# Kernel optimization log

Measured on AMD Instinct MI355X. Metric: run time of the kernel, lower is better.

The kernel has to match this reference:

```python
import jax, jax.numpy as jnp
import numpy as np
from jax import lax

B, CIN, COUT, K = 256, 3, 16, 3
D, H, W_ = 16, 32, 32
POOL = 4


def setup_inputs() -> dict:
    key = jax.random.key(0)
    kx, kw, kb = jax.random.split(key, 3)
    x = jax.random.normal(kx, (B, CIN, D, H, W_), dtype=jnp.float32)
    # Conv3d default init scale ~ 1/sqrt(fan_in)
    fan_in = CIN * K * K * K
    bound = 1.0 / np.sqrt(fan_in)
    W = jax.random.uniform(kw, (COUT, CIN, K, K, K), dtype=jnp.float32, minval=-bound, maxval=bound)
    b = jax.random.uniform(kb, (COUT,), dtype=jnp.float32, minval=-bound, maxval=bound)
    return {"x": x, "W": W, "b": b}


def reference(x, W, b):
    # Conv3d, valid padding, stride 1: [B,16,14,30,30]
    y = lax.conv_general_dilated(
        x, W, window_strides=(1, 1, 1), padding="VALID",
        dimension_numbers=("NCDHW", "OIDHW", "NCDHW"))
    y = y + b[None, :, None, None, None]
    # channel softmax (dim=1)
    s = jax.nn.softmax(y, axis=1)
    # 4x4x4 max-pool, stride 4, no padding: [B,16,3,7,7]
    out = lax.reduce_window(
        s, -jnp.inf, lax.max,
        window_dimensions=(1, 1, POOL, POOL, POOL),
        window_strides=(1, 1, POOL, POOL, POOL),
        padding="VALID")
    return out
```

## Files before the change

kernel.cpp:

```cpp
#include <hip/hip_runtime.h>
#include <math.h>

#define BATCH 256
#define CIN   3
#define COUT  16
#define DI    16
#define HI    32
#define WI    32

typedef _Float16 f16;
typedef f16   f16x4 __attribute__((ext_vector_type(4)));
typedef f16   f16x8 __attribute__((ext_vector_type(8)));
typedef float f32x4 __attribute__((ext_vector_type(4)));

#define LOG2E 1.44269504088896340736f

#define RS     72
#define PLANE  2160
#define XS_N   (6 * PLANE)
#define G8OFF  (2 * PLANE + 2 * RS)

#define SV8(a, b) __builtin_shufflevector(a, b, 0, 1, 2, 3, 4, 5, 6, 7)
#define MFMA16(A, B, C) __builtin_amdgcn_mfma_f32_16x16x32_f16(A, B, C, 0, 0, 0)

#define DPPMAX(v, ctrl) do {                                                  \
    int t_ = __builtin_amdgcn_update_dpp(                                     \
        0, __builtin_bit_cast(int, v), (ctrl), 0xF, 0xF, false);              \
    v = fmaxf(v, __builtin_bit_cast(float, t_));                              \
} while (0)

__global__ __launch_bounds__(256, 4) void conv_sm_pool_mfma(
    const float* __restrict__ x, const float* __restrict__ W,
    const float* __restrict__ bias, float* __restrict__ out)
{
    __shared__ __align__(16) f16 xs[XS_N];

    const int tid  = threadIdx.x;
    const int lane = tid & 63;
    const int wave = tid >> 6;

    const int wgid = blockIdx.x;
    const int r8 = wgid & 7;
    const int cw = (wgid >> 3) & 1;
    const int p  = ((wgid >> 4) << 3) + r8;
    const int b  = p / 3;
    const int pd = p % 3;
    const int d0 = pd * 4;

    const int col = lane & 15;
    const int kq  = lane >> 4;

    const float* wc  = W + col * 81;
    const float* wqp = wc + kq * 6;
    f16x8 wm[3];
    #pragma unroll
    for (int kw = 0; kw < 3; ++kw) {
        #pragma unroll
        for (int j = 0; j < 8; ++j) {
            const int ci = j & 3, jj = j >> 2;
            float v = (ci < 3) ? wqp[ci * 27 + 3 * jj + kw] * LOG2E : 0.f;
            wm[kw][j] = (f16)v;
        }
    }
    f16x8 wg = {};
    if (kq == 0) {
        #pragma unroll
        for (int j = 0; j < 8; ++j) {
            const int ci = j & 3, kw = j >> 2;
            if (ci < 3) wg[j] = (f16)(wc[ci * 27 + 24 + kw] * LOG2E);
        }
    } else if (kq == 1) {
        #pragma unroll
        for (int j = 0; j < 3; ++j) wg[j] = (f16)(wc[j * 27 + 26] * LOG2E);
    }
    const float4 braw = *(const float4*)(bias + kq * 4);
    float4 bv;
    bv.x = braw.x * LOG2E; bv.y = braw.y * LOG2E;
    bv.z = braw.z * LOG2E; bv.w = braw.w * LOG2E;

    if (cw == 0) {
        for (int i = tid; i < 900; i += 256) {
            int q = i % 5, r = i / 5;
            int hh = r % 30, dd = r / 30;
            const float* px = x + ((size_t)b * 48 + (d0 + dd)) * 1024 + hh * 32 + q * 4;
            float4 a0 = *(const float4*)(px);
            float4 a1 = *(const float4*)(px + 16384);
            float4 a2 = *(const float4*)(px + 32768);
            f16x8 p0, p1;
            p0[0] = (f16)a0.x; p0[1] = (f16)a1.x; p0[2] = (f16)a2.x; p0[3] = (f16)0.f;
            p0[4] = (f16)a0.y; p0[5] = (f16)a1.y; p0[6] = (f16)a2.y; p0[7] = (f16)0.f;
            p1[0] = (f16)a0.z; p1[1] = (f16)a1.z; p1[2] = (f16)a2.z; p1[3] = (f16)0.f;
            p1[4] = (f16)a0.w; p1[5] = (f16)a1.w; p1[6] = (f16)a2.w; p1[7] = (f16)0.f;
            f16* dst = xs + ((dd * 30 + hh) * 18 + q * 4) * 4;
            *(f16x8*)(dst) = p0;
            if (q < 4) *(f16x8*)(dst + 8) = p1;
        }
    } else {
        for (int i = tid; i < 720; i += 256) {
            int q = i & 3, r = i >> 2;
            int hh = r % 30, dd = r / 30;
            const float* px = x + ((size_t)b * 48 + (d0 + dd)) * 1024 + hh * 32 + 16 + q * 4;
            float4 a0 = *(const float4*)(px);
            float4 a1 = *(const float4*)(px + 16384);
            float4 a2 = *(const float4*)(px + 32768);
            f16x8 p0, p1;
            p0[0] = (f16)a0.x; p0[1] = (f16)a1.x; p0[2] = (f16)a2.x; p0[3] = (f16)0.f;
            p0[4] = (f16)a0.y; p0[5] = (f16)a1.y; p0[6] = (f16)a2.y; p0[7] = (f16)0.f;
            p1[0] = (f16)a0.z; p1[1] = (f16)a1.z; p1[2] = (f16)a2.z; p1[3] = (f16)0.f;
            p1[4] = (f16)a0.w; p1[5] = (f16)a1.w; p1[6] = (f16)a2.w; p1[7] = (f16)0.f;
            f16* dst = xs + ((dd * 30 + hh) * 18 + q * 4) * 4;
            *(f16x8*)(dst)     = p0;
            *(f16x8*)(dst + 8) = p1;
        }
    }

    const int g0   = kq * 2;
    const int off1 = (g0 / 3) * PLANE + (g0 % 3) * RS;
    const int off2 = ((g0 + 1) / 3) * PLANE + ((g0 + 1) % 3) * RS;
    const int hl = col >> 2, wl = col & 3;
    const int spat  = hl * RS + wl * 4;
    const int g8sel = (kq == 1) ? 8 : 0;

    __syncthreads();

    const int ncell = cw ? 21 : 28;
    for (int c = wave; c < ncell; c += 4) {
        int ch, pwl;
        if (cw == 0) { ch = c >> 2; pwl = c & 3; }
        else         { ch = c / 3;  pwl = c % 3; }
        const f16* base = xs + ch * 4 * RS + pwl * 16 + spat;
        const f16* a1 = base + off1;
        const f16* a2 = base + off2;
        const f16* a3 = base + G8OFF + g8sel;

        f16x4 Bv[4][8];
        #pragma unroll
        for (int d = 0; d < 4; ++d) {
            const int dp = d * PLANE;
            Bv[d][0] = *(const f16x4*)(a1 + dp);
            Bv[d][1] = *(const f16x4*)(a2 + dp);
            Bv[d][2] = *(const f16x4*)(a1 + dp + 4);
            Bv[d][3] = *(const f16x4*)(a2 + dp + 4);
            Bv[d][4] = *(const f16x4*)(a1 + dp + 8);
            Bv[d][5] = *(const f16x4*)(a2 + dp + 8);
            Bv[d][6] = *(const f16x4*)(a3 + dp);
            Bv[d][7] = *(const f16x4*)(a3 + dp + 4);
        }

        f32x4 acc[4];
        #pragma unroll
        for (int d = 0; d < 4; ++d) {
            f32x4 a_ = {0.f, 0.f, 0.f, 0.f};
            a_ = MFMA16(wm[0], SV8(Bv[d][0], Bv[d][1]), a_);
            a_ = MFMA16(wm[1], SV8(Bv[d][2], Bv[d][3]), a_);
            a_ = MFMA16(wm[2], SV8(Bv[d][4], Bv[d][5]), a_);
            a_ = MFMA16(wg,    SV8(Bv[d][6], Bv[d][7]), a_);
            acc[d] = a_;
        }
        __builtin_amdgcn_sched_group_barrier(0x100, 32, 0);
        __builtin_amdgcn_sched_group_barrier(0x008, 16, 0);

        float ev[4][4], s[4];
        #pragma unroll
        for (int d = 0; d < 4; ++d) {
            float y0 = acc[d][0] + bv.x, y1 = acc[d][1] + bv.y;
            float y2 = acc[d][2] + bv.z, y3 = acc[d][3] + bv.w;
            ev[d][0] = __builtin_amdgcn_exp2f(y0);
            ev[d][1] = __builtin_amdgcn_exp2f(y1);
            ev[d][2] = __builtin_amdgcn_exp2f(y2);
            ev[d][3] = __builtin_amdgcn_exp2f(y3);
            s[d] = (ev[d][0] + ev[d][1]) + (ev[d][2] + ev[d][3]);
        }
        #pragma unroll
        for (int d = 0; d < 4; ++d) s[d] += __shfl_xor(s[d], 16);
        #pragma unroll
        for (int d = 0; d < 4; ++d) s[d] += __shfl_xor(s[d], 32);

        f32x4 pm = {0.f, 0.f, 0.f, 0.f};
        #pragma unroll
        for (int d = 0; d < 4; ++d) {
            float iv = __builtin_amdgcn_rcpf(s[d]);
            pm[0] = fmaxf(pm[0], ev[d][0] * iv);
            pm[1] = fmaxf(pm[1], ev[d][1] * iv);
            pm[2] = fmaxf(pm[2], ev[d][2] * iv);
            pm[3] = fmaxf(pm[3], ev[d][3] * iv);
        }

        #pragma unroll
        for (int r = 0; r < 4; ++r) {
            float v = pm[r];
            DPPMAX(v, 0x128);
            DPPMAX(v, 0x124);
            DPPMAX(v, 0x122);
            DPPMAX(v, 0x121);
            pm[r] = v;
        }

        if (col == 0) {
            const int pw = cw ? 4 + pwl : pwl;
            float* po = out + ((size_t)b * COUT + kq * 4) * 147 + pd * 49 + ch * 7 + pw;
            po[0]   = pm[0];
            po[147] = pm[1];
            po[294] = pm[2];
            po[441] = pm[3];
        }
    }
}

extern "C" void kernel_launch(void* const* d_in, const int* in_sizes, int n_in,
                              void* d_out, int out_size, void* d_ws, size_t ws_size,
                              hipStream_t stream) {
    const float* x    = (const float*)d_in[0];
    const float* W    = (const float*)d_in[1];
    const float* bias = (const float*)d_in[2];
    float* out = (float*)d_out;

    conv_sm_pool_mfma<<<BATCH * 3 * 2, 256, 0, stream>>>(x, W, bias, out);
}
```

Baseline: 36.28 us.

## Merge width-split workgroups into one 512-thread block per depth slab

Replaces the two half-width workgroups per (batch, depth-slab) with a single 512-thread workgroup that stages the full 32-wide input slab in LDS and processes all 49 pooled cells across 8 waves. This removes the duplicated halo loads along width and the branchy split indexing, and drops the explicit MFMA/LDS scheduling barriers. The cost is doubled LDS per block (about 52 KB), which limits occupancy, and 49 cells over 8 waves leaves some waves with less work. The launch-bounds hint changes to 512 threads with a minimum of 6 blocks per CU.

```diff
diff --git a/kernel.cpp b/kernel.cpp
--- a/kernel.cpp
+++ b/kernel.cpp
@@ -15,10 +15,10 @@
 
 #define LOG2E 1.44269504088896340736f
 
-#define RS     72
-#define PLANE  2160
-#define XS_N   (6 * PLANE)
-#define G8OFF  (2 * PLANE + 2 * RS)
+#define ROWU   144
+#define PLANEU 4320
+#define XS_N   (6 * PLANEU)
+#define G8OFF  (2 * PLANEU + 2 * ROWU)
 
 #define SV8(a, b) __builtin_shufflevector(a, b, 0, 1, 2, 3, 4, 5, 6, 7)
 #define MFMA16(A, B, C) __builtin_amdgcn_mfma_f32_16x16x32_f16(A, B, C, 0, 0, 0)
@@ -29,7 +29,7 @@
     v = fmaxf(v, __builtin_bit_cast(float, t_));                              \
 } while (0)
 
-__global__ __launch_bounds__(256, 4) void conv_sm_pool_mfma(
+__global__ __launch_bounds__(512, 6) void conv_sm_pool_mfma(
     const float* __restrict__ x, const float* __restrict__ W,
     const float* __restrict__ bias, float* __restrict__ out)
 {
@@ -38,14 +38,9 @@
     const int tid  = threadIdx.x;
     const int lane = tid & 63;
     const int wave = tid >> 6;
-
-    const int wgid = blockIdx.x;
-    const int r8 = wgid & 7;
-    const int cw = (wgid >> 3) & 1;
-    const int p  = ((wgid >> 4) << 3) + r8;
-    const int b  = p / 3;
-    const int pd = p % 3;
-    const int d0 = pd * 4;
+    const int b    = blockIdx.x / 3;
+    const int pd   = blockIdx.x % 3;
+    const int d0   = pd * 4;
 
     const int col = lane & 15;
     const int kq  = lane >> 4;
@@ -78,57 +73,38 @@
     bv.x = braw.x * LOG2E; bv.y = braw.y * LOG2E;
     bv.z = braw.z * LOG2E; bv.w = braw.w * LOG2E;
 
-    if (cw == 0) {
-        for (int i = tid; i < 900; i += 256) {
-            int q = i % 5, r = i / 5;
-            int hh = r % 30, dd = r / 30;
-            const float* px = x + ((size_t)b * 48 + (d0 + dd)) * 1024 + hh * 32 + q * 4;
-            float4 a0 = *(const float4*)(px);
-            float4 a1 = *(const float4*)(px + 16384);
-            float4 a2 = *(const float4*)(px + 32768);
-            f16x8 p0, p1;
-            p0[0] = (f16)a0.x; p0[1] = (f16)a1.x; p0[2] = (f16)a2.x; p0[3] = (f16)0.f;
-            p0[4] = (f16)a0.y; p0[5] = (f16)a1.y; p0[6] = (f16)a2.y; p0[7] = (f16)0.f;
-            p1[0] = (f16)a0.z; p1[1] = (f16)a1.z; p1[2] = (f16)a2.z; p1[3] = (f16)0.f;
-            p1[4] = (f16)a0.w; p1[5] = (f16)a1.w; p1[6] = (f16)a2.w; p1[7] = (f16)0.f;
-            f16* dst = xs + ((dd * 30 + hh) * 18 + q * 4) * 4;
-            *(f16x8*)(dst) = p0;
-            if (q < 4) *(f16x8*)(dst + 8) = p1;
-        }
-    } else {
-        for (int i = tid; i < 720; i += 256) {
-            int q = i & 3, r = i >> 2;
-            int hh = r % 30, dd = r / 30;
-            const float* px = x + ((size_t)b * 48 + (d0 + dd)) * 1024 + hh * 32 + 16 + q * 4;
-            float4 a0 = *(const float4*)(px);
-            float4 a1 = *(const float4*)(px + 16384);
-            float4 a2 = *(const float4*)(px + 32768);
-            f16x8 p0, p1;
-            p0[0] = (f16)a0.x; p0[1] = (f16)a1.x; p0[2] = (f16)a2.x; p0[3] = (f16)0.f;
-            p0[4] = (f16)a0.y; p0[5] = (f16)a1.y; p0[6] = (f16)a2.y; p0[7] = (f16)0.f;
-            p1[0] = (f16)a0.z; p1[1] = (f16)a1.z; p1[2] = (f16)a2.z; p1[3] = (f16)0.f;
-            p1[4] = (f16)a0.w; p1[5] = (f16)a1.w; p1[6] = (f16)a2.w; p1[7] = (f16)0.f;
-            f16* dst = xs + ((dd * 30 + hh) * 18 + q * 4) * 4;
-            *(f16x8*)(dst)     = p0;
-            *(f16x8*)(dst + 8) = p1;
-        }
+    for (int i = tid; i < 1440; i += 512) {
+        int wqd = i & 7;
+        int r   = i >> 3;
+        int hh  = r % 30;
+        int dd  = r / 30;
+        const float* px = x + ((size_t)b * 48 + (d0 + dd)) * 1024 + hh * 32 + wqd * 4;
+        float4 a0 = *(const float4*)(px);
+        float4 a1 = *(const float4*)(px + 16384);
+        float4 a2 = *(const float4*)(px + 32768);
+        f16x8 p0, p1;
+        p0[0] = (f16)a0.x; p0[1] = (f16)a1.x; p0[2] = (f16)a2.x; p0[3] = (f16)0.f;
+        p0[4] = (f16)a0.y; p0[5] = (f16)a1.y; p0[6] = (f16)a2.y; p0[7] = (f16)0.f;
+        p1[0] = (f16)a0.z; p1[1] = (f16)a1.z; p1[2] = (f16)a2.z; p1[3] = (f16)0.f;
+        p1[4] = (f16)a0.w; p1[5] = (f16)a1.w; p1[6] = (f16)a2.w; p1[7] = (f16)0.f;
+        f16* dst = xs + ((dd * 30 + hh) * 36 + wqd * 4) * 4;
+        *(f16x8*)(dst)     = p0;
+        *(f16x8*)(dst + 8) = p1;
     }
 
     const int g0   = kq * 2;
-    const int off1 = (g0 / 3) * PLANE + (g0 % 3) * RS;
-    const int off2 = ((g0 + 1) / 3) * PLANE + ((g0 + 1) % 3) * RS;
+    const int off1 = (g0 / 3) * PLANEU + (g0 % 3) * ROWU;
+    const int off2 = ((g0 + 1) / 3) * PLANEU + ((g0 + 1) % 3) * ROWU;
     const int hl = col >> 2, wl = col & 3;
-    const int spat  = hl * RS + wl * 4;
-    const int g8sel = (kq == 1) ? 8 : 0;
+    const int spat  = hl * ROWU + wl * 4;
+    const int g8sel = (kq == 0) ? 0 : 8;
 
     __syncthreads();
 
-    const int ncell = cw ? 21 : 28;
-    for (int c = wave; c < ncell; c += 4) {
-        int ch, pwl;
-        if (cw == 0) { ch = c >> 2; pwl = c & 3; }
-        else         { ch = c / 3;  pwl = c % 3; }
-        const f16* base = xs + ch * 4 * RS + pwl * 16 + spat;
+    for (int c = wave; c < 49; c += 8) {
+        const int ch = c / 7;
+        const int pw = c - ch * 7;
+        const f16* base = xs + ch * 4 * ROWU + pw * 16 + spat;
         const f16* a1 = base + off1;
         const f16* a2 = base + off2;
         const f16* a3 = base + G8OFF + g8sel;
@@ -136,7 +112,7 @@
         f16x4 Bv[4][8];
         #pragma unroll
         for (int d = 0; d < 4; ++d) {
-            const int dp = d * PLANE;
+            const int dp = d * PLANEU;
             Bv[d][0] = *(const f16x4*)(a1 + dp);
             Bv[d][1] = *(const f16x4*)(a2 + dp);
             Bv[d][2] = *(const f16x4*)(a1 + dp + 4);
@@ -157,8 +133,6 @@
             a_ = MFMA16(wg,    SV8(Bv[d][6], Bv[d][7]), a_);
             acc[d] = a_;
         }
-        __builtin_amdgcn_sched_group_barrier(0x100, 32, 0);
-        __builtin_amdgcn_sched_group_barrier(0x008, 16, 0);
 
         float ev[4][4], s[4];
         #pragma unroll
@@ -197,8 +171,7 @@
         }
 
         if (col == 0) {
-            const int pw = cw ? 4 + pwl : pwl;
-            float* po = out + ((size_t)b * COUT + kq * 4) * 147 + pd * 49 + ch * 7 + pw;
+            float* po = out + ((size_t)b * COUT + kq * 4) * 147 + pd * 49 + c;
             po[0]   = pm[0];
             po[147] = pm[1];
             po[294] = pm[2];
@@ -215,5 +188,5 @@
     const float* bias = (const float*)d_in[2];
     float* out = (float*)d_out;
 
-    conv_sm_pool_mfma<<<BATCH * 3 * 2, 256, 0, stream>>>(x, W, bias, out);
+    conv_sm_pool_mfma<<<BATCH * 3, 512, 0, stream>>>(x, W, bias, out);
 }
```

New measurement: 30.29 us (median of 2 runs). -16.5%, faster.
